# Optimization experiments

Measured on AMD Instinct MI355X. Metric: run time of the kernel, lower is better.

Reference implementation:

```python
import jax, jax.numpy as jnp
import numpy as np

S = 64.0   # arcface scale
M = 0.5    # arcface additive angular margin
EPS = 1e-07
B, D, C = 1024, 512, 100000


def setup_inputs() -> dict:
    key = jax.random.key(0)
    k1, k2, k3 = jax.random.split(key, 3)
    features = jax.random.normal(k1, (B, D), dtype=jnp.float32)
    # Linear(512, 100000, bias=False) weight, ~1/sqrt(512) init scale.
    W = jax.random.normal(k2, (C, D), dtype=jnp.float32) * 0.04
    y_true = jax.random.randint(k3, (B,), 0, C, dtype=jnp.int64)
    return {"features": features, "W": W, "y_true": y_true}


def reference(features, W, y_true):
    # L2-normalize features along dim=1 (torch F.normalize, eps=1e-12).
    norm = jnp.maximum(jnp.linalg.norm(features, axis=1, keepdims=True), 1e-12)
    xn = features / norm
    # NOTE: the original module's weight-normalization loop is a no-op
    # (rebinds a local), so W is used unnormalized — faithful to the source.
    wf = xn @ W.T                                   # [B, C] cosine-like logits
    tgt = wf[jnp.arange(B), y_true]                  # true-class logit per row
    # arcface: s * cos(acos(clamp(t)) + m)
    numerator = S * jnp.cos(jnp.arccos(jnp.clip(tgt, -1.0 + EPS, 1.0 - EPS)) + M)
    # exp-sum over all classes except the true one (mask instead of python-loop concat)
    not_true = jnp.arange(C)[None, :] != y_true[:, None]   # [B, C]
    excl_sum = jnp.sum(jnp.where(not_true, jnp.exp(S * wf), 0.0), axis=1)
    denominator = jnp.exp(numerator) + excl_sum
    L = numerator - jnp.log(denominator)
    return -jnp.mean(L)
```

## Files before the change

kernel.cpp:

```cpp
#include <hip/hip_runtime.h>
#include <math.h>

#define BATCH 1024
#define DIM   512
#define NCLS  100000
#define SCALE_S 64.0f
#define MARGIN  0.5f
#define EPS_REF 1e-7f
#define SEXP 92.332482616893656878f

#define NSLAB 64
#define NBLK  1563
#define CHUNK 16
#define NCHUNK_WAVE 16

typedef __attribute__((ext_vector_type(4))) float floatx4;
typedef __attribute__((ext_vector_type(2))) long  longx2;

#if __has_builtin(__builtin_amdgcn_exp2f)
#define EXP2(x) __builtin_amdgcn_exp2f(x)
#else
#define EXP2(x) exp2f(x)
#endif

__device__ __forceinline__ float red16(float v) {
    v += __shfl_xor(v, 1);
    v += __shfl_xor(v, 2);
    v += __shfl_xor(v, 4);
    v += __shfl_xor(v, 8);
    return v;
}

__global__ __launch_bounds__(256)
void k_prep(const float* __restrict__ features,
            const float* __restrict__ W,
            const int* __restrict__ y,
            unsigned char* __restrict__ xf8,
            float* __restrict__ rowsum,
            float* __restrict__ tgt) {
    const int row = blockIdx.x;
    const int t = threadIdx.x;
    const int lane = t & 63;
    const int wave = t >> 6;
    __shared__ float redS[4], redD[4];

    const float2 v  = *(const float2*)(features + (size_t)row * DIM + t * 2);
    const float2 wv = *(const float2*)(W + (size_t)y[row] * DIM + t * 2);
    float ss = v.x * v.x + v.y * v.y;
    float dd = v.x * wv.x + v.y * wv.y;
    #pragma unroll
    for (int m = 32; m >= 1; m >>= 1) { ss += __shfl_xor(ss, m); dd += __shfl_xor(dd, m); }
    if (lane == 0) { redS[wave] = ss; redD[wave] = dd; }
    __syncthreads();
    const float tot  = redS[0] + redS[1] + redS[2] + redS[3];
    const float dtot = redD[0] + redD[1] + redD[2] + redD[3];
    const float nrm = fmaxf(sqrtf(tot), 1e-12f);
    const float sc = SEXP / nrm;

    int pk = __builtin_amdgcn_cvt_pk_fp8_f32(v.x * sc, v.y * sc, 0, false);
    const int k0 = t * 2;
    const int off = ((k0 & 31) >> 3) * 128 + (k0 >> 5) * 8 + (k0 & 7);
    *(unsigned short*)(xf8 + (size_t)row * DIM + off) = (unsigned short)(pk & 0xFFFF);

    if (t == 0) { rowsum[row] = 0.0f; tgt[row] = dtot / nrm; }
}


#define COMPUTE_CHUNK(Ab, c)                                                   \
    {                                                                          \
        floatx4 acc0 = (floatx4){0.f,0.f,0.f,0.f};                             \
        floatx4 acc1 = (floatx4){0.f,0.f,0.f,0.f};                             \
        floatx4 acc2 = (floatx4){0.f,0.f,0.f,0.f};                             \
        floatx4 acc3 = (floatx4){0.f,0.f,0.f,0.f};                             \
        _Pragma("unroll")                                                      \
        for (int kk = 0; kk < 16; ++kk) {                                      \
            const long av = (kk & 1) ? Ab[kk >> 1][1] : Ab[kk >> 1][0];        \
            acc0 = __builtin_amdgcn_mfma_f32_16x16x32_fp8_fp8(av, Bf[0][kk], acc0, 0, 0, 0); \
            acc1 = __builtin_amdgcn_mfma_f32_16x16x32_fp8_fp8(av, Bf[1][kk], acc1, 0, 0, 0); \
            acc2 = __builtin_amdgcn_mfma_f32_16x16x32_fp8_fp8(av, Bf[2][kk], acc2, 0, 0, 0); \
            acc3 = __builtin_amdgcn_mfma_f32_16x16x32_fp8_fp8(av, Bf[3][kk], acc3, 0, 0, 0); \
        }                                                                      \
        const int rowb = (wave * NCHUNK_WAVE + (c)) * CHUNK + quad * 4;        \
        _Pragma("unroll")                                                      \
        for (int reg = 0; reg < 4; ++reg) {                                    \
            float p;                                                           \
            if (full) {                                                        \
                p = EXP2(acc0[reg]) + EXP2(acc1[reg])                          \
                  + EXP2(acc2[reg]) + EXP2(acc3[reg]);                         \
            } else {                                                           \
                p = 0.f;                                                       \
                if (n0 +      l15 < NCLS) p += EXP2(acc0[reg]);                \
                if (n0 + 16 + l15 < NCLS) p += EXP2(acc1[reg]);                \
                if (n0 + 32 + l15 < NCLS) p += EXP2(acc2[reg]);                \
                if (n0 + 48 + l15 < NCLS) p += EXP2(acc3[reg]);                \
            }                                                                  \
            p = red16(p);                                                      \
            if (l15 == 0) atomicAdd(&rowsum[rowb + reg], p);                   \
        }                                                                      \
    }

__global__ __launch_bounds__(256, 2)
void k_gemm_fused(const float* __restrict__ W,
                  const unsigned char* __restrict__ xf8,
                  float* __restrict__ rowsum) {
    __shared__ __align__(16) unsigned char Ws[NSLAB * DIM];

    const int tid  = threadIdx.x;
    const int wave = tid >> 6;
    const int lane = tid & 63;
    const int quad = lane >> 4;
    const int l15  = lane & 15;
    const int n0   = blockIdx.x * NSLAB;

    #pragma unroll
    for (int j = 0; j < 8; ++j) {
        const int c  = j * 256 + tid;
        const int r  = c >> 5;
        const int cs = c & 31;
        int rg = n0 + r; if (rg > NCLS - 1) rg = NCLS - 1;
        const float4* s4 = (const float4*)(W + (size_t)rg * DIM + cs * 16);
        const float4 f0 = s4[0], f1 = s4[1], f2 = s4[2], f3 = s4[3];
        int w0 = __builtin_amdgcn_cvt_pk_fp8_f32(f0.x, f0.y, 0, false);
        w0     = __builtin_amdgcn_cvt_pk_fp8_f32(f0.z, f0.w, w0, true);
        int w1 = __builtin_amdgcn_cvt_pk_fp8_f32(f1.x, f1.y, 0, false);
        w1     = __builtin_amdgcn_cvt_pk_fp8_f32(f1.z, f1.w, w1, true);
        int w2 = __builtin_amdgcn_cvt_pk_fp8_f32(f2.x, f2.y, 0, false);
        w2     = __builtin_amdgcn_cvt_pk_fp8_f32(f2.z, f2.w, w2, true);
        int w3 = __builtin_amdgcn_cvt_pk_fp8_f32(f3.x, f3.y, 0, false);
        w3     = __builtin_amdgcn_cvt_pk_fp8_f32(f3.z, f3.w, w3, true);
        *(int4*)(&Ws[r * DIM + ((cs ^ (r & 7)) << 4)]) = make_int4(w0, w1, w2, w3);
    }
    __syncthreads();

    long Bf[4][16];
    #pragma unroll
    for (int ni = 0; ni < 4; ++ni) {
        const int r = ni * 16 + l15;
        #pragma unroll
        for (int kk = 0; kk < 16; ++kk) {
            const int cs = kk * 2 + (quad >> 1);
            Bf[ni][kk] = *(const long*)(&Ws[r * DIM + ((cs ^ (r & 7)) << 4) + ((quad & 1) << 3)]);
        }
    }

    const bool full = (n0 + NSLAB <= NCLS);

    const unsigned char* abase =
        xf8 + (size_t)(wave * NCHUNK_WAVE * CHUNK + l15) * DIM + quad * 128;

    longx2 A0[8], A1[8];
    #pragma unroll
    for (int j2 = 0; j2 < 8; ++j2)
        A0[j2] = *(const longx2*)(abase + j2 * 16);

    for (int c = 0; c < NCHUNK_WAVE; c += 2) {
        #pragma unroll
        for (int j2 = 0; j2 < 8; ++j2)
            A1[j2] = *(const longx2*)(abase + (size_t)(c + 1) * (CHUNK * DIM) + j2 * 16);
        COMPUTE_CHUNK(A0, c)
        const int cn = (c + 2 < NCHUNK_WAVE) ? c + 2 : 0;
        #pragma unroll
        for (int j2 = 0; j2 < 8; ++j2)
            A0[j2] = *(const longx2*)(abase + (size_t)cn * (CHUNK * DIM) + j2 * 16);
        COMPUTE_CHUNK(A1, c + 1)
    }
}

__global__ void k_finalize(const float* __restrict__ rowsum,
                           const float* __restrict__ tgt,
                           float* __restrict__ out) {
    const int tid = threadIdx.x;
    const int lane = tid & 63;
    const int wave = tid >> 6;
    __shared__ float red[4];

    float s = 0.f;
    #pragma unroll
    for (int i = 0; i < 4; ++i) {
        const int b = tid + i * 256;
        const float traw = tgt[b];
        const float tc = fminf(fmaxf(traw, -1.0f + EPS_REF), 1.0f - EPS_REF);
        const float num = SCALE_S * cosf(acosf(tc) + MARGIN);
        const float excl = rowsum[b] - expf(SCALE_S * traw);
        const float denom = expf(num) + excl;
        s += num - logf(denom);
    }
    #pragma unroll
    for (int m = 32; m >= 1; m >>= 1) s += __shfl_xor(s, m);
    if (lane == 0) red[wave] = s;
    __syncthreads();
    if (tid == 0)
        out[0] = -(red[0] + red[1] + red[2] + red[3]) / (float)BATCH;
}

extern "C" void kernel_launch(void* const* d_in, const int* in_sizes, int n_in,
                              void* d_out, int out_size, void* d_ws, size_t ws_size,
                              hipStream_t stream) {
    const float* features = (const float*)d_in[0];
    const float* W        = (const float*)d_in[1];
    const int*   y        = (const int*)d_in[2];
    float* out = (float*)d_out;

    const size_t XF8_BYTES = (size_t)BATCH * DIM;
    char* ws = (char*)d_ws;
    unsigned char* xf8 = (unsigned char*)ws;
    float* rowsum = (float*)(ws + XF8_BYTES);
    float* tgt    = (float*)(ws + XF8_BYTES + 4096);

    k_prep<<<BATCH, 256, 0, stream>>>(features, W, y, xf8, rowsum, tgt);
    k_gemm_fused<<<NBLK, 256, 0, stream>>>(W, xf8, rowsum);
    k_finalize<<<1, 256, 0, stream>>>(rowsum, tgt, out);
}
```

Measured before the change: 466.4 us.

## Spread rowsum atomics over eight copies and prefetch A before W staging

Row-sum accumulation is split across eight per-row copies selected by block index, and the finalize kernel adds the copies together. This is meant to reduce atomic contention on the same addresses from the many blocks. The first A-fragment load is also issued before the W slab conversion so it overlaps, and the chunk loop is kept rolled with macro-expanded bodies. The cost is a larger workspace, eight times the zeroing in prep, and extra reads in finalize.

New measurement: 396.4 us. 15.0% less time.

```diff
diff --git a/kernel.cpp b/kernel.cpp
--- a/kernel.cpp
+++ b/kernel.cpp
@@ -13,6 +13,7 @@
 #define NBLK  1563
 #define CHUNK 16
 #define NCHUNK_WAVE 16
+#define NRSCOPY 8
 
 typedef __attribute__((ext_vector_type(4))) float floatx4;
 typedef __attribute__((ext_vector_type(2))) long  longx2;
@@ -62,42 +63,52 @@
     const int off = ((k0 & 31) >> 3) * 128 + (k0 >> 5) * 8 + (k0 & 7);
     *(unsigned short*)(xf8 + (size_t)row * DIM + off) = (unsigned short)(pk & 0xFFFF);
 
-    if (t == 0) { rowsum[row] = 0.0f; tgt[row] = dtot / nrm; }
-}
-
-
-#define COMPUTE_CHUNK(Ab, c)                                                   \
-    {                                                                          \
-        floatx4 acc0 = (floatx4){0.f,0.f,0.f,0.f};                             \
-        floatx4 acc1 = (floatx4){0.f,0.f,0.f,0.f};                             \
-        floatx4 acc2 = (floatx4){0.f,0.f,0.f,0.f};                             \
-        floatx4 acc3 = (floatx4){0.f,0.f,0.f,0.f};                             \
-        _Pragma("unroll")                                                      \
-        for (int kk = 0; kk < 16; ++kk) {                                      \
-            const long av = (kk & 1) ? Ab[kk >> 1][1] : Ab[kk >> 1][0];        \
-            acc0 = __builtin_amdgcn_mfma_f32_16x16x32_fp8_fp8(av, Bf[0][kk], acc0, 0, 0, 0); \
-            acc1 = __builtin_amdgcn_mfma_f32_16x16x32_fp8_fp8(av, Bf[1][kk], acc1, 0, 0, 0); \
-            acc2 = __builtin_amdgcn_mfma_f32_16x16x32_fp8_fp8(av, Bf[2][kk], acc2, 0, 0, 0); \
-            acc3 = __builtin_amdgcn_mfma_f32_16x16x32_fp8_fp8(av, Bf[3][kk], acc3, 0, 0, 0); \
-        }                                                                      \
-        const int rowb = (wave * NCHUNK_WAVE + (c)) * CHUNK + quad * 4;        \
-        _Pragma("unroll")                                                      \
-        for (int reg = 0; reg < 4; ++reg) {                                    \
-            float p;                                                           \
-            if (full) {                                                        \
-                p = EXP2(acc0[reg]) + EXP2(acc1[reg])                          \
-                  + EXP2(acc2[reg]) + EXP2(acc3[reg]);                         \
-            } else {                                                           \
-                p = 0.f;                                                       \
-                if (n0 +      l15 < NCLS) p += EXP2(acc0[reg]);                \
-                if (n0 + 16 + l15 < NCLS) p += EXP2(acc1[reg]);                \
-                if (n0 + 32 + l15 < NCLS) p += EXP2(acc2[reg]);                \
-                if (n0 + 48 + l15 < NCLS) p += EXP2(acc3[reg]);                \
-            }                                                                  \
-            p = red16(p);                                                      \
-            if (l15 == 0) atomicAdd(&rowsum[rowb + reg], p);                   \
-        }                                                                      \
-    }
+    if (t < NRSCOPY) rowsum[t * BATCH + row] = 0.0f;
+    if (t == 0) tgt[row] = dtot / nrm;
+}
+
+
+#define LBK(ni,kk) { const int r_ = (ni)*16 + l15;                             \
+    const int cs_ = (kk)*2 + qh;                                               \
+    Bf[ni][kk] = *(const long*)(&Ws[r_*DIM + (((cs_)^(r_&7))<<4) + ql8]); }
+
+#define LB16(ni) LBK(ni,0) LBK(ni,1) LBK(ni,2)  LBK(ni,3)  LBK(ni,4)  LBK(ni,5)  LBK(ni,6)  LBK(ni,7) \
+                 LBK(ni,8) LBK(ni,9) LBK(ni,10) LBK(ni,11) LBK(ni,12) LBK(ni,13) LBK(ni,14) LBK(ni,15)
+
+#define LA(Ab, c) { const unsigned char* p_ = abase + (size_t)(c) * (CHUNK * DIM); \
+    Ab[0] = *(const longx2*)(p_ +  0); Ab[1] = *(const longx2*)(p_ + 16);      \
+    Ab[2] = *(const longx2*)(p_ + 32); Ab[3] = *(const longx2*)(p_ + 48);      \
+    Ab[4] = *(const longx2*)(p_ + 64); Ab[5] = *(const longx2*)(p_ + 80);      \
+    Ab[6] = *(const longx2*)(p_ + 96); Ab[7] = *(const longx2*)(p_ + 112); }
+
+#define STEP(Ab, kk) { const long av_ = Ab[(kk)>>1][(kk)&1];                   \
+    acc0 = __builtin_amdgcn_mfma_f32_16x16x32_fp8_fp8(av_, Bf[0][kk], acc0, 0, 0, 0); \
+    acc1 = __builtin_amdgcn_mfma_f32_16x16x32_fp8_fp8(av_, Bf[1][kk], acc1, 0, 0, 0); \
+    acc2 = __builtin_amdgcn_mfma_f32_16x16x32_fp8_fp8(av_, Bf[2][kk], acc2, 0, 0, 0); \
+    acc3 = __builtin_amdgcn_mfma_f32_16x16x32_fp8_fp8(av_, Bf[3][kk], acc3, 0, 0, 0); }
+
+#define EPI(reg) { float p_;                                                   \
+    if (full) { p_ = EXP2(acc0[reg]) + EXP2(acc1[reg])                         \
+                   + EXP2(acc2[reg]) + EXP2(acc3[reg]); }                      \
+    else { p_ = 0.f;                                                           \
+        if (n0 +      l15 < NCLS) p_ += EXP2(acc0[reg]);                       \
+        if (n0 + 16 + l15 < NCLS) p_ += EXP2(acc1[reg]);                       \
+        if (n0 + 32 + l15 < NCLS) p_ += EXP2(acc2[reg]);                       \
+        if (n0 + 48 + l15 < NCLS) p_ += EXP2(acc3[reg]); }                     \
+    p_ = red16(p_);                                                            \
+    if (l15 == 0) atomicAdd(&rs[rowb_ + (reg)], p_); }
+
+#define COMPUTE(Ab, c) {                                                       \
+    floatx4 acc0 = (floatx4){0.f,0.f,0.f,0.f};                                 \
+    floatx4 acc1 = (floatx4){0.f,0.f,0.f,0.f};                                 \
+    floatx4 acc2 = (floatx4){0.f,0.f,0.f,0.f};                                 \
+    floatx4 acc3 = (floatx4){0.f,0.f,0.f,0.f};                                 \
+    STEP(Ab,0)  STEP(Ab,1)  STEP(Ab,2)  STEP(Ab,3)                             \
+    STEP(Ab,4)  STEP(Ab,5)  STEP(Ab,6)  STEP(Ab,7)                             \
+    STEP(Ab,8)  STEP(Ab,9)  STEP(Ab,10) STEP(Ab,11)                            \
+    STEP(Ab,12) STEP(Ab,13) STEP(Ab,14) STEP(Ab,15)                            \
+    const int rowb_ = (wave * NCHUNK_WAVE + (c)) * CHUNK + quad * 4;           \
+    EPI(0) EPI(1) EPI(2) EPI(3) }
 
 __global__ __launch_bounds__(256, 2)
 void k_gemm_fused(const float* __restrict__ W,
@@ -110,7 +121,16 @@
     const int lane = tid & 63;
     const int quad = lane >> 4;
     const int l15  = lane & 15;
+    const int qh   = quad >> 1;
+    const int ql8  = (quad & 1) << 3;
     const int n0   = blockIdx.x * NSLAB;
+    float* rs = rowsum + (blockIdx.x & (NRSCOPY - 1)) * BATCH;
+
+    const unsigned char* abase =
+        xf8 + (size_t)(wave * NCHUNK_WAVE * CHUNK + l15) * DIM + quad * 128;
+
+    longx2 A0[8], A1[8];
+    LA(A0, 0)
 
     #pragma unroll
     for (int j = 0; j < 8; ++j) {
@@ -133,36 +153,17 @@
     __syncthreads();
 
     long Bf[4][16];
-    #pragma unroll
-    for (int ni = 0; ni < 4; ++ni) {
-        const int r = ni * 16 + l15;
-        #pragma unroll
-        for (int kk = 0; kk < 16; ++kk) {
-            const int cs = kk * 2 + (quad >> 1);
-            Bf[ni][kk] = *(const long*)(&Ws[r * DIM + ((cs ^ (r & 7)) << 4) + ((quad & 1) << 3)]);
-        }
-    }
+    LB16(0) LB16(1) LB16(2) LB16(3)
 
     const bool full = (n0 + NSLAB <= NCLS);
 
-    const unsigned char* abase =
-        xf8 + (size_t)(wave * NCHUNK_WAVE * CHUNK + l15) * DIM + quad * 128;
-
-    longx2 A0[8], A1[8];
-    #pragma unroll
-    for (int j2 = 0; j2 < 8; ++j2)
-        A0[j2] = *(const longx2*)(abase + j2 * 16);
-
+    #pragma unroll 1
     for (int c = 0; c < NCHUNK_WAVE; c += 2) {
-        #pragma unroll
-        for (int j2 = 0; j2 < 8; ++j2)
-            A1[j2] = *(const longx2*)(abase + (size_t)(c + 1) * (CHUNK * DIM) + j2 * 16);
-        COMPUTE_CHUNK(A0, c)
+        LA(A1, c + 1)
+        COMPUTE(A0, c)
         const int cn = (c + 2 < NCHUNK_WAVE) ? c + 2 : 0;
-        #pragma unroll
-        for (int j2 = 0; j2 < 8; ++j2)
-            A0[j2] = *(const longx2*)(abase + (size_t)cn * (CHUNK * DIM) + j2 * 16);
-        COMPUTE_CHUNK(A1, c + 1)
+        LA(A0, cn)
+        COMPUTE(A1, c + 1)
     }
 }
 
@@ -178,10 +179,13 @@
     #pragma unroll
     for (int i = 0; i < 4; ++i) {
         const int b = tid + i * 256;
+        float rsum = 0.f;
+        #pragma unroll
+        for (int cp = 0; cp < NRSCOPY; ++cp) rsum += rowsum[cp * BATCH + b];
         const float traw = tgt[b];
         const float tc = fminf(fmaxf(traw, -1.0f + EPS_REF), 1.0f - EPS_REF);
         const float num = SCALE_S * cosf(acosf(tc) + MARGIN);
-        const float excl = rowsum[b] - expf(SCALE_S * traw);
+        const float excl = rsum - expf(SCALE_S * traw);
         const float denom = expf(num) + excl;
         s += num - logf(denom);
     }
@@ -202,10 +206,11 @@
     float* out = (float*)d_out;
 
     const size_t XF8_BYTES = (size_t)BATCH * DIM;
+    const size_t RS_BYTES  = (size_t)NRSCOPY * BATCH * sizeof(float);
     char* ws = (char*)d_ws;
     unsigned char* xf8 = (unsigned char*)ws;
     float* rowsum = (float*)(ws + XF8_BYTES);
-    float* tgt    = (float*)(ws + XF8_BYTES + 4096);
+    float* tgt    = (float*)(ws + XF8_BYTES + RS_BYTES);
 
     k_prep<<<BATCH, 256, 0, stream>>>(features, W, y, xf8, rowsum, tgt);
     k_gemm_fused<<<NBLK, 256, 0, stream>>>(W, xf8, rowsum);
```
